# Kernel optimization log

Hardware: AMD Instinct MI355X
Metric: run time of the kernel (lower is better)

The kernel has to match this reference:

```python
import jax, jax.numpy as jnp
import numpy as np

B, O, I, D = 8, 128, 128, 1024


def setup_inputs() -> dict:
    key = jax.random.key(0)
    ks = jax.random.split(key, 10)
    s = 1.0 / np.sqrt(2 * D)  # torch Linear default-ish scale
    return {
        "output": jax.random.normal(ks[0], (B, O, D), jnp.float32),
        "context": jax.random.normal(ks[1], (B, I, D), jnp.float32),
        "mask": jax.random.randint(ks[2], (B, I), 0, 2, jnp.int32),
        # self.w = Linear(2*dim, dim), split into the output-half and context-half
        "w_out_w": jax.random.normal(ks[3], (D, D), jnp.float32) * s,
        "w_ctx_w": jax.random.normal(ks[4], (D, D), jnp.float32) * s,
        "w_b": jax.random.normal(ks[5], (D,), jnp.float32) * s,
        # self.score = Linear(dim, 1)
        "score_w": jax.random.normal(ks[6], (D,), jnp.float32) * (1.0 / np.sqrt(D)),
        "score_b": jnp.zeros((), jnp.float32),
        # self.linear_out = Linear(2*dim, dim)
        "lin_w": jax.random.normal(ks[7], (2 * D, D), jnp.float32) * s,
        "lin_b": jax.random.normal(ks[8], (D,), jnp.float32) * s,
    }


def reference(output, context, mask, w_out_w, w_ctx_w, w_b, score_w, score_b, lin_w, lin_b):
    # Additive (Bahdanau) attention.
    # cat(out, ctx) @ W^T == out @ W1 + ctx @ W2  -> avoid [B,O,I,2D] concat.
    s_out = jnp.einsum('bod,de->boe', output, w_out_w)            # [B,O,D]
    s_ctx = jnp.einsum('bid,de->bie', context, w_ctx_w)           # [B,I,D]
    h = jax.nn.leaky_relu(s_out[:, :, None, :] + s_ctx[:, None, :, :] + w_b)  # [B,O,I,D]
    score = jnp.einsum('boid,d->boi', h, score_w) + score_b       # [B,O,I]
    score = jnp.where(mask[:, None, :] == 1, -jnp.inf, score)
    attn = jax.nn.softmax(score, axis=-1)                         # [B,O,I]
    attn_output = jnp.einsum('boi,bid->bod', attn, context)       # mix=True: bmm
    # fn=True: linear_out on cat(attn_output, output) then leaky_relu
    combined = jnp.concatenate([attn_output, output], axis=-1)    # [B,O,2D]
    attn_output = jax.nn.leaky_relu(combined @ lin_w + lin_b)     # [B,O,D]
    return attn_output, attn
```

## Files before the change

kernel.cpp:

```cpp
#include <hip/hip_runtime.h>

namespace {

constexpr int kB = 8, kO = 128, kI = 128, kD = 1024;
constexpr long kOutAttnOff = (long)kB * kO * kD;

typedef __attribute__((ext_vector_type(8))) short short8;
typedef __attribute__((ext_vector_type(4))) float f32x4;
typedef __attribute__((ext_vector_type(2))) float f32x2;
typedef __attribute__((ext_vector_type(2))) unsigned u32x2;

__device__ __forceinline__ float leaky(float x) { return fmaxf(x, 0.01f * x); }

__device__ __forceinline__ short f2bf(float f) {
    unsigned u = __builtin_bit_cast(unsigned, f);
    u += 0x7FFFu + ((u >> 16) & 1u);
    return (short)(u >> 16);
}
__device__ __forceinline__ void b8tofs(const short8 v, float* f) {
    const unsigned* u = (const unsigned*)&v;
#pragma unroll
    for (int j = 0; j < 4; ++j) {
        f[2 * j]     = __builtin_bit_cast(float, u[j] << 16);
        f[2 * j + 1] = __builtin_bit_cast(float, u[j] & 0xffff0000u);
    }
}
__device__ __forceinline__ void bpair(const short8 a, const short8 b, f32x2* p) {
    float fa[8], fb[8];
    b8tofs(a, fa); b8tofs(b, fb);
#pragma unroll
    for (int j = 0; j < 8; ++j) p[j] = f32x2{fa[j], fb[j]};
}
__device__ __forceinline__ f32x2 vabs2(f32x2 x) {
    u32x2 u = __builtin_bit_cast(u32x2, x);
    u &= 0x7fffffffu;
    return __builtin_bit_cast(f32x2, u);
}

__device__ __forceinline__ void gll16(const void* g, void* l) {
    __builtin_amdgcn_global_load_lds(
        (const __attribute__((address_space(1))) int*)g,
        (__attribute__((address_space(3))) int*)l, 16, 0, 0);
}

__global__ __launch_bounds__(256)
void conv_all(const float* __restrict__ output, const float* __restrict__ context,
              const float* __restrict__ w1, const float* __restrict__ w2,
              const float* __restrict__ lin,
              short* __restrict__ ob16, short* __restrict__ cb16,
              short* __restrict__ w1t, short* __restrict__ w2t,
              short* __restrict__ lint)
{
    __shared__ float T[64][68];
    const int bid = blockIdx.x, tid = threadIdx.x;

    if (bid < 1024) {
        const int idx = bid * 256 + tid;
        const float* src; short* dst; int i;
        if (idx < (1 << 17)) { src = output;  dst = ob16; i = idx; }
        else                 { src = context; dst = cb16; i = idx - (1 << 17); }
        const float4* s4 = (const float4*)src + (long)i * 2;
        const float4 v0 = s4[0], v1 = s4[1];
        short8 r;
        r[0] = f2bf(v0.x); r[1] = f2bf(v0.y); r[2] = f2bf(v0.z); r[3] = f2bf(v0.w);
        r[4] = f2bf(v1.x); r[5] = f2bf(v1.y); r[6] = f2bf(v1.z); r[7] = f2bf(v1.w);
        *(short8*)(dst + (long)i * 8) = r;
        return;
    }

    const int tb = bid - 1024;
    const float* src; short* dst; long C, R; int t2;
    if (tb < 256)      { src = w1;  dst = w1t;  R = 1024; C = 1024; t2 = tb; }
    else if (tb < 512) { src = w2;  dst = w2t;  R = 1024; C = 1024; t2 = tb - 256; }
    else               { src = lin; dst = lint; R = 2048; C = 1024; t2 = tb - 512; }
    const int tr = t2 >> 4, tc = t2 & 15;
    const int r = tid >> 2, q = tid & 3;

    const float* s = src + (long)(tr * 64 + r) * C + tc * 64 + q * 16;
    const float4 a0 = ((const float4*)s)[0];
    const float4 a1 = ((const float4*)s)[1];
    const float4 a2 = ((const float4*)s)[2];
    const float4 a3 = ((const float4*)s)[3];
    *(float4*)&T[r][q * 16 + 0]  = a0;
    *(float4*)&T[r][q * 16 + 4]  = a1;
    *(float4*)&T[r][q * 16 + 8]  = a2;
    *(float4*)&T[r][q * 16 + 12] = a3;
    __syncthreads();

    short8 o0, o1;
#pragma unroll
    for (int j = 0; j < 8; ++j)  o0[j] = f2bf(T[q * 16 + j][r]);
#pragma unroll
    for (int j = 0; j < 8; ++j)  o1[j] = f2bf(T[q * 16 + 8 + j][r]);
    short* dp = dst + (long)(tc * 64 + r) * R + tr * 64 + q * 16;
    *(short8*)dp       = o0;
    *((short8*)dp + 1) = o1;
}

__global__ __launch_bounds__(256, 4)
void mm_jobs(const short* __restrict__ ob16, const short* __restrict__ cb16,
             const short* __restrict__ w1t, const short* __restrict__ w2t,
             const short* __restrict__ lint,
             const float* __restrict__ w_b, const float* __restrict__ lin_b,
             float* __restrict__ s_out, short* __restrict__ s_ctx16,
             float* __restrict__ outlin, short* __restrict__ ctxlin)
{
    __shared__ short As[2][64][64];
    __shared__ short Bs[2][64][64];
    const int tid = threadIdx.x;
    const int t = (blockIdx.x & 7) * 128 + (blockIdx.x >> 3);
    const int lane = tid & 63, w = tid >> 6;

    const short *Ap, *Bp;
    int lda, ldb, bm, bn, ldc;
    const float* bias = nullptr;
    float* Cf = nullptr;
    short* Ch = nullptr;

    if (t < 768) {
        const int job = t >> 8, tl = t & 255;
        bm = (tl & 15) * 64;
        bn = (tl >> 4) * 64;
        lda = 1024; ldb = 1024; ldc = 1024;
        if (job == 0)      { Ap = ob16; Bp = w1t;         bias = w_b;   Cf = s_out;   }
        else if (job == 1) { Ap = ob16; Bp = lint + 1024; ldb = 2048; bias = lin_b; Cf = outlin; }
        else               { Ap = cb16; Bp = w2t;                       Ch = s_ctx16; }
    } else {
        const int tl = t - 768, bz = tl >> 5, t2 = tl & 31;
        bm = (t2 & 15) * 64;
        bn = (t2 >> 4) * 64;
        Ap = lint; lda = 2048;
        Bp = cb16 + (long)bz * (kI * kD); ldb = 1024;
        Ch = ctxlin + (long)bz * (kD * kI); ldc = 128;
    }

    const int m0 = (w >> 1) * 32, n0 = (w & 1) * 32;
    const int fr = lane & 15, fcol = lane >> 4, sl = lane & 7;
    const int r8 = lane >> 3;
    const int sw8 = ((lane & 7) ^ r8) * 8;
    const int w16 = w * 16;

    f32x4 acc[2][2] = {};

    auto stage = [&](int buf, int k0) {
        const short* ga = Ap + (long)(bm + w16 + r8) * lda + k0 + sw8;
        gll16(ga,                 &As[buf][w16][0]);
        gll16(ga + 8 * (long)lda, &As[buf][w16 + 8][0]);
        const short* gb = Bp + (long)(bn + w16 + r8) * ldb + k0 + sw8;
        gll16(gb,                 &Bs[buf][w16][0]);
        gll16(gb + 8 * (long)ldb, &Bs[buf][w16 + 8][0]);
    };

    stage(0, 0);
    __syncthreads();
    int cur = 0;
    for (int s = 0; s < 16; ++s) {
        if (s < 15) stage(cur ^ 1, (s + 1) << 6);
#pragma unroll
        for (int ks8 = 0; ks8 < 8; ks8 += 4) {
            const int sa = ((ks8 + fcol) ^ sl) * 8;
            short8 a[2], b[2];
#pragma unroll
            for (int mi = 0; mi < 2; ++mi)
                a[mi] = *(const short8*)&As[cur][m0 + mi * 16 + fr][sa];
#pragma unroll
            for (int ni = 0; ni < 2; ++ni)
                b[ni] = *(const short8*)&Bs[cur][n0 + ni * 16 + fr][sa];
#pragma unroll
            for (int mi = 0; mi < 2; ++mi)
#pragma unroll
                for (int ni = 0; ni < 2; ++ni)
                    acc[mi][ni] = __builtin_amdgcn_mfma_f32_16x16x32_bf16(
                        a[mi], b[ni], acc[mi][ni], 0, 0, 0);
        }
        __syncthreads();
        cur ^= 1;
    }

    float bv[2] = {0, 0};
    if (bias) {
#pragma unroll
        for (int ni = 0; ni < 2; ++ni) bv[ni] = bias[bn + n0 + ni * 16 + fr];
    }
#pragma unroll
    for (int mi = 0; mi < 2; ++mi)
#pragma unroll
        for (int ni = 0; ni < 2; ++ni)
#pragma unroll
            for (int r = 0; r < 4; ++r) {
                const int row = bm + m0 + mi * 16 + ((lane >> 4) << 2) + r;
                const int col = bn + n0 + ni * 16 + fr;
                const float v = acc[mi][ni][r] + bv[ni];
                if (Ch) Ch[(long)row * ldc + col] = f2bf(v);
                else    Cf[(long)row * ldc + col] = v;
            }
}

__global__ __launch_bounds__(256, 3)
void score_final(const float* __restrict__ s_out, const short* __restrict__ s_ctx16,
                 const float* __restrict__ score_w, const float* __restrict__ score_b,
                 const int* __restrict__ mask, const short* __restrict__ ctxlin,
                 const float* __restrict__ outlin, float* __restrict__ out_main,
                 float* __restrict__ attn_f32)
{
    __shared__ float As[2][1032];
    __shared__ __align__(16) char CsPool[32768];
    __shared__ short Wsh[1032];
    __shared__ float Ps[4][2][128];
    __shared__ float Psi[4][128];
    __shared__ float so_sh[2];
    __shared__ int   Msk[128];
    __shared__ __align__(16) short Pl[16][136];

    short* CsS = (short*)CsPool;
    const int b   = blockIdx.x;
    const int o0  = blockIdx.y * 2;
    const int tid = threadIdx.x;
    const int wv  = tid >> 6;
    const int ln  = tid & 63;
    const int fr  = ln & 15, fg = ln >> 4;

    const short* crow = s_ctx16 + (long)b * kI * kD;
    auto stageCs = [&](int slot, int dc) {
#pragma unroll
        for (int it = 0; it < 4; ++it) {
            const int rb = wv * 32 + it * 8;
            const int r  = rb + (ln >> 3);
            const int sc = (ln & 7) ^ (r & 7);
            gll16(crow + (long)r * kD + dc + sc * 8, CsS + slot * 8192 + rb * 64);
        }
    };

    stageCs(0, 0);

    const float* arow = s_out + (long)(b * kO + o0) * kD;
#pragma unroll
    for (int q = 0; q < 2; ++q) {
        const int tq = tid + q * 256;
        const int rr = tq >> 8, c4 = (tq & 255) * 4;
        *(float4*)&As[rr][c4] = *(const float4*)&arow[(long)rr * kD + c4];
    }
    {
        const float4 w4 = *(const float4*)&score_w[tid * 4];
        const unsigned p0 = (unsigned)(unsigned short)f2bf(w4.x)
                          | ((unsigned)(unsigned short)f2bf(w4.y) << 16);
        const unsigned p1 = (unsigned)(unsigned short)f2bf(w4.z)
                          | ((unsigned)(unsigned short)f2bf(w4.w) << 16);
        *(u32x2*)&Wsh[tid * 4] = u32x2{p0, p1};
    }
    if (tid < 128) Msk[tid] = mask[b * kI + tid];
    {
        short* pf = &Pl[0][0];
        for (int j = tid; j < 272; j += 256) *(short8*)(pf + j * 8) = short8{};
    }
    __syncthreads();

    if (wv < 2) {
        const short8 wA = *(const short8*)&Wsh[ln * 16];
        const short8 wB = *(const short8*)&Wsh[ln * 16 + 8];
        float wf[16];
        b8tofs(wA, wf); b8tofs(wB, wf + 8);
        float acc = 0.0f;
#pragma unroll
        for (int q = 0; q < 4; ++q) {
            const float4 av = *(const float4*)&As[wv][ln * 16 + q * 4];
            acc = fmaf(av.x, wf[q*4+0], acc); acc = fmaf(av.y, wf[q*4+1], acc);
            acc = fmaf(av.z, wf[q*4+2], acc); acc = fmaf(av.w, wf[q*4+3], acc);
        }
#pragma unroll
        for (int d = 1; d < 64; d <<= 1) acc += __shfl_xor(acc, d, 64);
        if (ln == 0) so_sh[wv] = acc;
    }

    f32x2 si2{0.0f, 0.0f};
    f32x2 sa2[2] = {f32x2{0.0f, 0.0f}, f32x2{0.0f, 0.0f}};
    const int kb = wv * 16;

    int buf = 0;
    for (int c = 0; c < 16; ++c) {
        const int dc = c * 64;
        if (c < 15) stageCs(buf ^ 1, dc + 64);
        const short* Cb = CsS + buf * 8192;
        const int sc0 = ((wv * 2 + 0) ^ (ln & 7)) * 8;
        const int sc1 = ((wv * 2 + 1) ^ (ln & 7)) * 8;
        const short8 cA0 = *(const short8*)&Cb[ln * 64 + sc0];
        const short8 cA1 = *(const short8*)&Cb[ln * 64 + sc1];
        const short8 cB0 = *(const short8*)&Cb[(ln + 64) * 64 + sc0];
        const short8 cB1 = *(const short8*)&Cb[(ln + 64) * 64 + sc1];
        f32x2 c2[16];
        bpair(cA0, cB0, c2);
        bpair(cA1, cB1, c2 + 8);
        const short8 w0 = *(const short8*)&Wsh[dc + kb];
        const short8 w1 = *(const short8*)&Wsh[dc + kb + 8];
        float wr[16];
        b8tofs(w0, wr); b8tofs(w1, wr + 8);
        float av0[16], av1[16];
#pragma unroll
        for (int q = 0; q < 4; ++q) {
            *(float4*)&av0[q * 4] = *(const float4*)&As[0][dc + kb + q * 4];
            *(float4*)&av1[q * 4] = *(const float4*)&As[1][dc + kb + q * 4];
        }
#pragma unroll
        for (int d = 0; d < 16; ++d) {
            const f32x2 w2 = {wr[d], wr[d]};
            si2 += c2[d] * w2;
            const f32x2 x0 = c2[d] + f32x2{av0[d], av0[d]};
            const f32x2 x1 = c2[d] + f32x2{av1[d], av1[d]};
            sa2[0] += vabs2(x0) * w2;
            sa2[1] += vabs2(x1) * w2;
        }
        __syncthreads();
        buf ^= 1;
    }

    short* Bsh = (short*)CsPool;
    const short* ctxb = ctxlin + (long)b * (kD * kI);
    auto stageB = [&](int half, int nc) {
#pragma unroll
        for (int it = 0; it < 4; ++it) {
            const int rb = wv * 16 + it * 4;
            const int r  = rb + (ln >> 4);
            const int n  = nc * 64 + r;
            const int sc = (ln & 15) ^ (r & 7);
            gll16(ctxb + (long)n * kI + sc * 8, Bsh + half * 8192 + rb * kI);
        }
    };
    stageB(0, 0);

#pragma unroll
    for (int o = 0; o < 2; ++o) {
        Ps[wv][o][ln]      = sa2[o].x;
        Ps[wv][o][ln + 64] = sa2[o].y;
    }
    Psi[wv][ln]      = si2.x;
    Psi[wv][ln + 64] = si2.y;
    __syncthreads();

    if (wv < 2) {
        const int ow = wv;
        const float negInf = -__builtin_huge_valf();
        const float sb = score_b[0];
        const float siT0 = Psi[0][ln] + Psi[1][ln] + Psi[2][ln] + Psi[3][ln];
        const float siT1 = Psi[0][ln + 64] + Psi[1][ln + 64]
                         + Psi[2][ln + 64] + Psi[3][ln + 64];
        const float saT0 = Ps[0][ow][ln] + Ps[1][ow][ln]
                         + Ps[2][ow][ln] + Ps[3][ow][ln];
        const float saT1 = Ps[0][ow][ln + 64] + Ps[1][ow][ln + 64]
                         + Ps[2][ow][ln + 64] + Ps[3][ow][ln + 64];
        const float soV = so_sh[ow];
        float s0 = 0.505f * (soV + siT0) + 0.495f * saT0 + sb;
        float s1 = 0.505f * (soV + siT1) + 0.495f * saT1 + sb;
        if (Msk[ln]      != 0) s0 = negInf;
        if (Msk[ln + 64] != 0) s1 = negInf;

        float m = fmaxf(s0, s1);
#pragma unroll
        for (int d = 1; d < 64; d <<= 1) m = fmaxf(m, __shfl_xor(m, d, 64));
        const float e0 = __expf(s0 - m);
        const float e1 = __expf(s1 - m);
        float sum = e0 + e1;
#pragma unroll
        for (int d = 1; d < 64; d <<= 1) sum += __shfl_xor(sum, d, 64);
        const float inv = 1.0f / sum;

        const long rowoff = (long)(b * kO + o0 + ow) * kI;
        const float p0 = e0 * inv, p1 = e1 * inv;
        attn_f32[rowoff + ln]      = p0;
        attn_f32[rowoff + ln + 64] = p1;
        Pl[ow][ln]      = f2bf(p0);
        Pl[ow][ln + 64] = f2bf(p1);
    }
    __syncthreads();

    int half = 0;
    for (int nc = 0; nc < 16; ++nc) {
        if (nc < 15) stageB(half ^ 1, nc + 1);
        const short* Bc = Bsh + half * 8192;
        f32x4 acc{};
#pragma unroll
        for (int ks = 0; ks < 4; ++ks) {
            const short8 a = *(const short8*)&Pl[fr][ks * 32 + fg * 8];
            const int sc = ((ks * 4 + fg) ^ (fr & 7)) * 8;
            const short8 bb = *(const short8*)&Bc[(wv * 16 + fr) * kI + sc];
            acc = __builtin_amdgcn_mfma_f32_16x16x32_bf16(a, bb, acc, 0, 0, 0);
        }
        if (fg == 0) {
#pragma unroll
            for (int r = 0; r < 2; ++r) {
                const int n = nc * 64 + wv * 16 + fr;
                const long off = (long)(b * kO + o0 + r) * kD + n;
                out_main[off] = leaky(acc[r] + outlin[off]);
            }
        }
        __syncthreads();
        half ^= 1;
    }
}

}

extern "C" void kernel_launch(void* const* d_in, const int* in_sizes, int n_in,
                              void* d_out, int out_size, void* d_ws, size_t ws_size,
                              hipStream_t stream)
{
    const float* output  = (const float*)d_in[0];
    const float* context = (const float*)d_in[1];
    const int*   mask    = (const int*)d_in[2];
    const float* w_out_w = (const float*)d_in[3];
    const float* w_ctx_w = (const float*)d_in[4];
    const float* w_b     = (const float*)d_in[5];
    const float* score_w = (const float*)d_in[6];
    const float* score_b = (const float*)d_in[7];
    const float* lin_w   = (const float*)d_in[8];
    const float* lin_b   = (const float*)d_in[9];

    float* out_main = (float*)d_out;
    float* out_attn = out_main + kOutAttnOff;
    float* s_out    = out_main;

    char* wp = (char*)d_ws;
    short* s_ctx16 = (short*)wp;  wp += (size_t)2 << 20;
    short* ob16    = (short*)wp;  wp += (size_t)2 << 20;
    short* cb16    = (short*)wp;  wp += (size_t)2 << 20;
    short* w1t     = (short*)wp;  wp += (size_t)2 << 20;
    short* w2t     = (short*)wp;  wp += (size_t)2 << 20;
    short* lint    = (short*)wp;  wp += (size_t)4 << 20;
    float* outlin  = (float*)wp;  wp += (size_t)4 << 20;
    short* ctxlin  = (short*)wp;

    const dim3 blk(256);

    hipLaunchKernelGGL(conv_all, dim3(2048), blk, 0, stream,
        output, context, w_out_w, w_ctx_w, lin_w, ob16, cb16, w1t, w2t, lint);

    hipLaunchKernelGGL(mm_jobs, dim3(1024), blk, 0, stream,
        ob16, cb16, w1t, w2t, lint, w_b, lin_b, s_out, s_ctx16, outlin, ctxlin);

    hipLaunchKernelGGL(score_final, dim3(8, 64), blk, 0, stream,
        s_out, s_ctx16, score_w, score_b, mask, ctxlin, outlin, out_main, out_attn);
}
```

Baseline: 60.90 us.

## Compact unmasked context rows and skip score work for masked positions

Builds a compacted index list of unmasked context positions with ballot and popcount, then gathers only those rows into shared memory. When at most 64 positions are unmasked, a half-width path stages and processes only 64 rows, roughly halving the score-loop loads and FLOPs. Masked scores are set to -inf directly. This adds a ballot pass, an extra barrier and an indirect gather, and the speedup depends on the mask density of the inputs.

After: 61.42 us. Within noise of the previous version (+0.9%).

```diff
diff --git a/kernel.cpp b/kernel.cpp
--- a/kernel.cpp
+++ b/kernel.cpp
@@ -210,6 +210,8 @@
     __shared__ float Psi[4][128];
     __shared__ float so_sh[2];
     __shared__ int   Msk[128];
+    __shared__ unsigned long long Mball[2];
+    __shared__ int   Idx[128];
     __shared__ __align__(16) short Pl[16][136];
 
     short* CsS = (short*)CsPool;
@@ -220,18 +222,12 @@
     const int ln  = tid & 63;
     const int fr  = ln & 15, fg = ln >> 4;
 
-    const short* crow = s_ctx16 + (long)b * kI * kD;
-    auto stageCs = [&](int slot, int dc) {
-#pragma unroll
-        for (int it = 0; it < 4; ++it) {
-            const int rb = wv * 32 + it * 8;
-            const int r  = rb + (ln >> 3);
-            const int sc = (ln & 7) ^ (r & 7);
-            gll16(crow + (long)r * kD + dc + sc * 8, CsS + slot * 8192 + rb * 64);
-        }
-    };
-
-    stageCs(0, 0);
+    int mv = 1;
+    if (tid < 128) { mv = mask[b * kI + tid]; Msk[tid] = mv; }
+    if (wv < 2) {
+        const unsigned long long bal = __ballot(mv == 0);
+        if (ln == 0) Mball[wv] = bal;
+    }
 
     const float* arow = s_out + (long)(b * kO + o0) * kD;
 #pragma unroll
@@ -248,12 +244,47 @@
                           | ((unsigned)(unsigned short)f2bf(w4.w) << 16);
         *(u32x2*)&Wsh[tid * 4] = u32x2{p0, p1};
     }
-    if (tid < 128) Msk[tid] = mask[b * kI + tid];
     {
         short* pf = &Pl[0][0];
         for (int j = tid; j < 272; j += 256) *(short8*)(pf + j * 8) = short8{};
     }
     __syncthreads();
+
+    const unsigned long long m0 = Mball[0], m1 = Mball[1];
+    const int K0 = __popcll(m0);
+    const int K  = K0 + __popcll(m1);
+    if (tid < 128) {
+        if (mv == 0) {
+            const int cp = (tid < 64)
+                ? __popcll(m0 & ((1ull << tid) - 1))
+                : K0 + __popcll(m1 & ((1ull << (tid - 64)) - 1));
+            Idx[cp] = tid;
+        }
+        if (tid >= K) Idx[tid] = 0;
+    }
+    __syncthreads();
+
+    const short* crow = s_ctx16 + (long)b * kI * kD;
+    auto stageCs64 = [&](int slot, int dc) {
+#pragma unroll
+        for (int it = 0; it < 2; ++it) {
+            const int rb = wv * 16 + it * 8;
+            const int r  = rb + (ln >> 3);
+            const int sc = (ln & 7) ^ (r & 7);
+            gll16(crow + (long)Idx[r] * kD + dc + sc * 8, CsS + slot * 8192 + rb * 64);
+        }
+    };
+    auto stageCsF = [&](int slot, int dc) {
+#pragma unroll
+        for (int it = 0; it < 4; ++it) {
+            const int rb = wv * 32 + it * 8;
+            const int r  = rb + (ln >> 3);
+            const int sc = (ln & 7) ^ (r & 7);
+            gll16(crow + (long)Idx[r] * kD + dc + sc * 8, CsS + slot * 8192 + rb * 64);
+        }
+    };
+
+    if (K <= 64) stageCs64(0, 0); else stageCsF(0, 0);
 
     if (wv < 2) {
         const short8 wA = *(const short8*)&Wsh[ln * 16];
@@ -271,46 +302,90 @@
         for (int d = 1; d < 64; d <<= 1) acc += __shfl_xor(acc, d, 64);
         if (ln == 0) so_sh[wv] = acc;
     }
-
-    f32x2 si2{0.0f, 0.0f};
-    f32x2 sa2[2] = {f32x2{0.0f, 0.0f}, f32x2{0.0f, 0.0f}};
+    __syncthreads();
+
     const int kb = wv * 16;
 
-    int buf = 0;
-    for (int c = 0; c < 16; ++c) {
-        const int dc = c * 64;
-        if (c < 15) stageCs(buf ^ 1, dc + 64);
-        const short* Cb = CsS + buf * 8192;
-        const int sc0 = ((wv * 2 + 0) ^ (ln & 7)) * 8;
-        const int sc1 = ((wv * 2 + 1) ^ (ln & 7)) * 8;
-        const short8 cA0 = *(const short8*)&Cb[ln * 64 + sc0];
-        const short8 cA1 = *(const short8*)&Cb[ln * 64 + sc1];
-        const short8 cB0 = *(const short8*)&Cb[(ln + 64) * 64 + sc0];
-        const short8 cB1 = *(const short8*)&Cb[(ln + 64) * 64 + sc1];
-        f32x2 c2[16];
-        bpair(cA0, cB0, c2);
-        bpair(cA1, cB1, c2 + 8);
-        const short8 w0 = *(const short8*)&Wsh[dc + kb];
-        const short8 w1 = *(const short8*)&Wsh[dc + kb + 8];
-        float wr[16];
-        b8tofs(w0, wr); b8tofs(w1, wr + 8);
-        float av0[16], av1[16];
-#pragma unroll
-        for (int q = 0; q < 4; ++q) {
-            *(float4*)&av0[q * 4] = *(const float4*)&As[0][dc + kb + q * 4];
-            *(float4*)&av1[q * 4] = *(const float4*)&As[1][dc + kb + q * 4];
-        }
-#pragma unroll
-        for (int d = 0; d < 16; ++d) {
-            const f32x2 w2 = {wr[d], wr[d]};
-            si2 += c2[d] * w2;
-            const f32x2 x0 = c2[d] + f32x2{av0[d], av0[d]};
-            const f32x2 x1 = c2[d] + f32x2{av1[d], av1[d]};
-            sa2[0] += vabs2(x0) * w2;
-            sa2[1] += vabs2(x1) * w2;
-        }
-        __syncthreads();
-        buf ^= 1;
+    if (K <= 64) {
+        float si = 0.0f, sa0 = 0.0f, sa1 = 0.0f;
+        int buf = 0;
+        for (int c = 0; c < 16; ++c) {
+            const int dc = c * 64;
+            if (c < 15) stageCs64(buf ^ 1, dc + 64);
+            const short* Cb = CsS + buf * 8192;
+            const int sc0 = ((wv * 2 + 0) ^ (ln & 7)) * 8;
+            const int sc1 = ((wv * 2 + 1) ^ (ln & 7)) * 8;
+            const short8 cA0 = *(const short8*)&Cb[ln * 64 + sc0];
+            const short8 cA1 = *(const short8*)&Cb[ln * 64 + sc1];
+            float cf[16];
+            b8tofs(cA0, cf); b8tofs(cA1, cf + 8);
+            const short8 w0 = *(const short8*)&Wsh[dc + kb];
+            const short8 w1 = *(const short8*)&Wsh[dc + kb + 8];
+            float wr[16];
+            b8tofs(w0, wr); b8tofs(w1, wr + 8);
+            float av0[16], av1[16];
+#pragma unroll
+            for (int q = 0; q < 4; ++q) {
+                *(float4*)&av0[q * 4] = *(const float4*)&As[0][dc + kb + q * 4];
+                *(float4*)&av1[q * 4] = *(const float4*)&As[1][dc + kb + q * 4];
+            }
+#pragma unroll
+            for (int d = 0; d < 16; ++d) {
+                si  = fmaf(cf[d], wr[d], si);
+                sa0 = fmaf(__builtin_fabsf(av0[d] + cf[d]), wr[d], sa0);
+                sa1 = fmaf(__builtin_fabsf(av1[d] + cf[d]), wr[d], sa1);
+            }
+            __syncthreads();
+            buf ^= 1;
+        }
+        Psi[wv][ln]    = si;
+        Ps[wv][0][ln]  = sa0;
+        Ps[wv][1][ln]  = sa1;
+    } else {
+        f32x2 si2{0.0f, 0.0f};
+        f32x2 sa2[2] = {f32x2{0.0f, 0.0f}, f32x2{0.0f, 0.0f}};
+        int buf = 0;
+        for (int c = 0; c < 16; ++c) {
+            const int dc = c * 64;
+            if (c < 15) stageCsF(buf ^ 1, dc + 64);
+            const short* Cb = CsS + buf * 8192;
+            const int sc0 = ((wv * 2 + 0) ^ (ln & 7)) * 8;
+            const int sc1 = ((wv * 2 + 1) ^ (ln & 7)) * 8;
+            const short8 cA0 = *(const short8*)&Cb[ln * 64 + sc0];
+            const short8 cA1 = *(const short8*)&Cb[ln * 64 + sc1];
+            const short8 cB0 = *(const short8*)&Cb[(ln + 64) * 64 + sc0];
+            const short8 cB1 = *(const short8*)&Cb[(ln + 64) * 64 + sc1];
+            f32x2 c2[16];
+            bpair(cA0, cB0, c2);
+            bpair(cA1, cB1, c2 + 8);
+            const short8 w0 = *(const short8*)&Wsh[dc + kb];
+            const short8 w1 = *(const short8*)&Wsh[dc + kb + 8];
+            float wr[16];
+            b8tofs(w0, wr); b8tofs(w1, wr + 8);
+            float av0[16], av1[16];
+#pragma unroll
+            for (int q = 0; q < 4; ++q) {
+                *(float4*)&av0[q * 4] = *(const float4*)&As[0][dc + kb + q * 4];
+                *(float4*)&av1[q * 4] = *(const float4*)&As[1][dc + kb + q * 4];
+            }
+#pragma unroll
+            for (int d = 0; d < 16; ++d) {
+                const f32x2 w2 = {wr[d], wr[d]};
+                si2 += c2[d] * w2;
+                const f32x2 x0 = c2[d] + f32x2{av0[d], av0[d]};
+                const f32x2 x1 = c2[d] + f32x2{av1[d], av1[d]};
+                sa2[0] += vabs2(x0) * w2;
+                sa2[1] += vabs2(x1) * w2;
+            }
+            __syncthreads();
+            buf ^= 1;
+        }
+        Psi[wv][ln]         = si2.x;
+        Psi[wv][ln + 64]    = si2.y;
+        Ps[wv][0][ln]       = sa2[0].x;
+        Ps[wv][0][ln + 64]  = sa2[0].y;
+        Ps[wv][1][ln]       = sa2[1].x;
+        Ps[wv][1][ln + 64]  = sa2[1].y;
     }
 
     short* Bsh = (short*)CsPool;
@@ -326,32 +401,28 @@
         }
     };
     stageB(0, 0);
-
-#pragma unroll
-    for (int o = 0; o < 2; ++o) {
-        Ps[wv][o][ln]      = sa2[o].x;
-        Ps[wv][o][ln + 64] = sa2[o].y;
-    }
-    Psi[wv][ln]      = si2.x;
-    Psi[wv][ln + 64] = si2.y;
     __syncthreads();
 
     if (wv < 2) {
         const int ow = wv;
         const float negInf = -__builtin_huge_valf();
         const float sb = score_b[0];
-        const float siT0 = Psi[0][ln] + Psi[1][ln] + Psi[2][ln] + Psi[3][ln];
-        const float siT1 = Psi[0][ln + 64] + Psi[1][ln + 64]
-                         + Psi[2][ln + 64] + Psi[3][ln + 64];
-        const float saT0 = Ps[0][ow][ln] + Ps[1][ow][ln]
-                         + Ps[2][ow][ln] + Ps[3][ow][ln];
-        const float saT1 = Ps[0][ow][ln + 64] + Ps[1][ow][ln + 64]
-                         + Ps[2][ow][ln + 64] + Ps[3][ow][ln + 64];
         const float soV = so_sh[ow];
-        float s0 = 0.505f * (soV + siT0) + 0.495f * saT0 + sb;
-        float s1 = 0.505f * (soV + siT1) + 0.495f * saT1 + sb;
-        if (Msk[ln]      != 0) s0 = negInf;
-        if (Msk[ln + 64] != 0) s1 = negInf;
+        float s0 = negInf, s1 = negInf;
+        if (Msk[ln] == 0) {
+            const int j = __popcll(m0 & ((1ull << ln) - 1));
+            const float siT = Psi[0][j] + Psi[1][j] + Psi[2][j] + Psi[3][j];
+            const float saT = Ps[0][ow][j] + Ps[1][ow][j]
+                            + Ps[2][ow][j] + Ps[3][ow][j];
+            s0 = 0.505f * (soV + siT) + 0.495f * saT + sb;
+        }
+        if (Msk[ln + 64] == 0) {
+            const int j = K0 + __popcll(m1 & ((1ull << ln) - 1));
+            const float siT = Psi[0][j] + Psi[1][j] + Psi[2][j] + Psi[3][j];
+            const float saT = Ps[0][ow][j] + Ps[1][ow][j]
+                            + Ps[2][ow][j] + Ps[3][ow][j];
+            s1 = 0.505f * (soV + siT) + 0.495f * saT + sb;
+        }
 
         float m = fmaxf(s0, s1);
 #pragma unroll
```

## Fuse fp32-to-bf16 conversion and weight transpose into the GEMM kernel

Applied to the files above, without the earlier changes.

Removes the separate conversion/transpose kernel and has the GEMM load fp32 activations and weights directly, converting to bf16 and transposing through a shared-memory staging tile each k-step. This removes a kernel launch and the round-trip of bf16 copies through global memory. In exchange, every GEMM tile re-converts and re-transposes the same weight data many times, and each k-step gains extra syncs plus register-held prefetch in place of async LDS loads. The launch bound also drops to 3 blocks per SIMD.

Result: slower. 77.03 us (+26.5%).

```diff
diff --git a/kernel.cpp b/kernel.cpp
--- a/kernel.cpp
+++ b/kernel.cpp
@@ -36,6 +36,12 @@
     u &= 0x7fffffffu;
     return __builtin_bit_cast(f32x2, u);
 }
+__device__ __forceinline__ short8 pack8(const float4 a, const float4 b) {
+    short8 r;
+    r[0] = f2bf(a.x); r[1] = f2bf(a.y); r[2] = f2bf(a.z); r[3] = f2bf(a.w);
+    r[4] = f2bf(b.x); r[5] = f2bf(b.y); r[6] = f2bf(b.z); r[7] = f2bf(b.w);
+    return r;
+}
 
 __device__ __forceinline__ void gll16(const void* g, void* l) {
     __builtin_amdgcn_global_load_lds(
@@ -43,119 +49,113 @@
         (__attribute__((address_space(3))) int*)l, 16, 0, 0);
 }
 
-__global__ __launch_bounds__(256)
-void conv_all(const float* __restrict__ output, const float* __restrict__ context,
-              const float* __restrict__ w1, const float* __restrict__ w2,
-              const float* __restrict__ lin,
-              short* __restrict__ ob16, short* __restrict__ cb16,
-              short* __restrict__ w1t, short* __restrict__ w2t,
-              short* __restrict__ lint)
-{
-    __shared__ float T[64][68];
-    const int bid = blockIdx.x, tid = threadIdx.x;
-
-    if (bid < 1024) {
-        const int idx = bid * 256 + tid;
-        const float* src; short* dst; int i;
-        if (idx < (1 << 17)) { src = output;  dst = ob16; i = idx; }
-        else                 { src = context; dst = cb16; i = idx - (1 << 17); }
-        const float4* s4 = (const float4*)src + (long)i * 2;
-        const float4 v0 = s4[0], v1 = s4[1];
-        short8 r;
-        r[0] = f2bf(v0.x); r[1] = f2bf(v0.y); r[2] = f2bf(v0.z); r[3] = f2bf(v0.w);
-        r[4] = f2bf(v1.x); r[5] = f2bf(v1.y); r[6] = f2bf(v1.z); r[7] = f2bf(v1.w);
-        *(short8*)(dst + (long)i * 8) = r;
-        return;
-    }
-
-    const int tb = bid - 1024;
-    const float* src; short* dst; long C, R; int t2;
-    if (tb < 256)      { src = w1;  dst = w1t;  R = 1024; C = 1024; t2 = tb; }
-    else if (tb < 512) { src = w2;  dst = w2t;  R = 1024; C = 1024; t2 = tb - 256; }
-    else               { src = lin; dst = lint; R = 2048; C = 1024; t2 = tb - 512; }
-    const int tr = t2 >> 4, tc = t2 & 15;
-    const int r = tid >> 2, q = tid & 3;
-
-    const float* s = src + (long)(tr * 64 + r) * C + tc * 64 + q * 16;
-    const float4 a0 = ((const float4*)s)[0];
-    const float4 a1 = ((const float4*)s)[1];
-    const float4 a2 = ((const float4*)s)[2];
-    const float4 a3 = ((const float4*)s)[3];
-    *(float4*)&T[r][q * 16 + 0]  = a0;
-    *(float4*)&T[r][q * 16 + 4]  = a1;
-    *(float4*)&T[r][q * 16 + 8]  = a2;
-    *(float4*)&T[r][q * 16 + 12] = a3;
-    __syncthreads();
-
-    short8 o0, o1;
-#pragma unroll
-    for (int j = 0; j < 8; ++j)  o0[j] = f2bf(T[q * 16 + j][r]);
-#pragma unroll
-    for (int j = 0; j < 8; ++j)  o1[j] = f2bf(T[q * 16 + 8 + j][r]);
-    short* dp = dst + (long)(tc * 64 + r) * R + tr * 64 + q * 16;
-    *(short8*)dp       = o0;
-    *((short8*)dp + 1) = o1;
-}
-
-__global__ __launch_bounds__(256, 4)
-void mm_jobs(const short* __restrict__ ob16, const short* __restrict__ cb16,
-             const short* __restrict__ w1t, const short* __restrict__ w2t,
-             const short* __restrict__ lint,
-             const float* __restrict__ w_b, const float* __restrict__ lin_b,
-             float* __restrict__ s_out, short* __restrict__ s_ctx16,
-             float* __restrict__ outlin, short* __restrict__ ctxlin)
+__global__ __launch_bounds__(256, 3)
+void mm_all(const float* __restrict__ output, const float* __restrict__ context,
+            const float* __restrict__ w1, const float* __restrict__ w2,
+            const float* __restrict__ lin,
+            const float* __restrict__ w_b, const float* __restrict__ lin_b,
+            float* __restrict__ s_out, short* __restrict__ s_ctx16,
+            float* __restrict__ outlin, short* __restrict__ ctxlin)
 {
     __shared__ short As[2][64][64];
     __shared__ short Bs[2][64][64];
+    __shared__ float Tf[64][65];
+
     const int tid = threadIdx.x;
     const int t = (blockIdx.x & 7) * 128 + (blockIdx.x >> 3);
     const int lane = tid & 63, w = tid >> 6;
 
-    const short *Ap, *Bp;
-    int lda, ldb, bm, bn, ldc;
+    const float *Dsrc, *Tsrc;
+    int R0, C0, bm, bn, ldc;
     const float* bias = nullptr;
     float* Cf = nullptr;
     short* Ch = nullptr;
+    bool transA = false;
 
     if (t < 768) {
         const int job = t >> 8, tl = t & 255;
         bm = (tl & 15) * 64;
         bn = (tl >> 4) * 64;
-        lda = 1024; ldb = 1024; ldc = 1024;
-        if (job == 0)      { Ap = ob16; Bp = w1t;         bias = w_b;   Cf = s_out;   }
-        else if (job == 1) { Ap = ob16; Bp = lint + 1024; ldb = 2048; bias = lin_b; Cf = outlin; }
-        else               { Ap = cb16; Bp = w2t;                       Ch = s_ctx16; }
+        ldc = 1024; R0 = bm; C0 = bn;
+        if (job == 0)      { Dsrc = output;  Tsrc = w1;  bias = w_b;   Cf = s_out;   }
+        else if (job == 1) { Dsrc = output;  Tsrc = lin + (long)1024 * 1024;
+                             bias = lin_b;  Cf = outlin; }
+        else               { Dsrc = context; Tsrc = w2;  Ch = s_ctx16; }
     } else {
         const int tl = t - 768, bz = tl >> 5, t2 = tl & 31;
         bm = (t2 & 15) * 64;
         bn = (t2 >> 4) * 64;
-        Ap = lint; lda = 2048;
-        Bp = cb16 + (long)bz * (kI * kD); ldb = 1024;
+        Dsrc = context + (long)bz * (kI * kD); R0 = bn;
+        Tsrc = lin; C0 = bm;
         Ch = ctxlin + (long)bz * (kD * kI); ldc = 128;
+        transA = true;
     }
 
     const int m0 = (w >> 1) * 32, n0 = (w & 1) * 32;
     const int fr = lane & 15, fcol = lane >> 4, sl = lane & 7;
     const int r8 = lane >> 3;
-    const int sw8 = ((lane & 7) ^ r8) * 8;
+    const int c8 = lane & 7;
     const int w16 = w * 16;
 
     f32x4 acc[2][2] = {};
 
-    auto stage = [&](int buf, int k0) {
-        const short* ga = Ap + (long)(bm + w16 + r8) * lda + k0 + sw8;
-        gll16(ga,                 &As[buf][w16][0]);
-        gll16(ga + 8 * (long)lda, &As[buf][w16 + 8][0]);
-        const short* gb = Bp + (long)(bn + w16 + r8) * ldb + k0 + sw8;
-        gll16(gb,                 &Bs[buf][w16][0]);
-        gll16(gb + 8 * (long)ldb, &Bs[buf][w16 + 8][0]);
-    };
-
-    stage(0, 0);
+    float4 dv[4], tv[4];
+    auto loadDirect = [&](int k0) {
+        const float* g = Dsrc + (long)(R0 + w16 + r8) * kD + k0 + ((c8 ^ r8) * 8);
+        dv[0] = ((const float4*)g)[0];
+        dv[1] = ((const float4*)g)[1];
+        const float* g2 = g + 8 * kD;
+        dv[2] = ((const float4*)g2)[0];
+        dv[3] = ((const float4*)g2)[1];
+    };
+    auto loadTrans = [&](int k0) {
+#pragma unroll
+        for (int p = 0; p < 4; ++p) {
+            const int f = tid + p * 256;
+            const int row = f >> 4, colq = (f & 15) * 4;
+            tv[p] = *(const float4*)&Tsrc[(long)(k0 + row) * 1024 + C0 + colq];
+        }
+    };
+    auto writeDirect = [&](short (*dst)[64]) {
+        *(short8*)&dst[w16 + r8][c8 * 8]     = pack8(dv[0], dv[1]);
+        *(short8*)&dst[w16 + 8 + r8][c8 * 8] = pack8(dv[2], dv[3]);
+    };
+    auto writeTf = [&]() {
+#pragma unroll
+        for (int p = 0; p < 4; ++p) {
+            const int f = tid + p * 256;
+            const int row = f >> 4, colq = (f & 15) * 4;
+            Tf[row][colq + 0] = tv[p].x;
+            Tf[row][colq + 1] = tv[p].y;
+            Tf[row][colq + 2] = tv[p].z;
+            Tf[row][colq + 3] = tv[p].w;
+        }
+    };
+    auto transToDst = [&](short (*dst)[64]) {
+#pragma unroll
+        for (int h = 0; h < 2; ++h) {
+            const int n = w16 + h * 8 + r8;
+            const int kc = (c8 ^ r8) * 8;
+            float4 a, b;
+            a.x = Tf[kc + 0][n]; a.y = Tf[kc + 1][n];
+            a.z = Tf[kc + 2][n]; a.w = Tf[kc + 3][n];
+            b.x = Tf[kc + 4][n]; b.y = Tf[kc + 5][n];
+            b.z = Tf[kc + 6][n]; b.w = Tf[kc + 7][n];
+            *(short8*)&dst[n][c8 * 8] = pack8(a, b);
+        }
+    };
+
+    loadDirect(0);
+    loadTrans(0);
+    writeTf();
+    writeDirect(transA ? Bs[0] : As[0]);
     __syncthreads();
+    transToDst(transA ? As[0] : Bs[0]);
+    __syncthreads();
+
     int cur = 0;
     for (int s = 0; s < 16; ++s) {
-        if (s < 15) stage(cur ^ 1, (s + 1) << 6);
+        if (s < 15) { loadDirect((s + 1) << 6); loadTrans((s + 1) << 6); }
 #pragma unroll
         for (int ks8 = 0; ks8 < 8; ks8 += 4) {
             const int sa = ((ks8 + fcol) ^ sl) * 8;
@@ -173,8 +173,16 @@
                     acc[mi][ni] = __builtin_amdgcn_mfma_f32_16x16x32_bf16(
                         a[mi], b[ni], acc[mi][ni], 0, 0, 0);
         }
-        __syncthreads();
-        cur ^= 1;
+        if (s < 15) {
+            const int nxt = cur ^ 1;
+            __syncthreads();
+            writeTf();
+            writeDirect(transA ? Bs[nxt] : As[nxt]);
+            __syncthreads();
+            transToDst(transA ? As[nxt] : Bs[nxt]);
+            __syncthreads();
+            cur = nxt;
+        }
     }
 
     float bv[2] = {0, 0};
@@ -420,21 +428,14 @@
 
     char* wp = (char*)d_ws;
     short* s_ctx16 = (short*)wp;  wp += (size_t)2 << 20;
-    short* ob16    = (short*)wp;  wp += (size_t)2 << 20;
-    short* cb16    = (short*)wp;  wp += (size_t)2 << 20;
-    short* w1t     = (short*)wp;  wp += (size_t)2 << 20;
-    short* w2t     = (short*)wp;  wp += (size_t)2 << 20;
-    short* lint    = (short*)wp;  wp += (size_t)4 << 20;
     float* outlin  = (float*)wp;  wp += (size_t)4 << 20;
     short* ctxlin  = (short*)wp;
 
     const dim3 blk(256);
 
-    hipLaunchKernelGGL(conv_all, dim3(2048), blk, 0, stream,
-        output, context, w_out_w, w_ctx_w, lin_w, ob16, cb16, w1t, w2t, lint);
-
-    hipLaunchKernelGGL(mm_jobs, dim3(1024), blk, 0, stream,
-        ob16, cb16, w1t, w2t, lint, w_b, lin_b, s_out, s_ctx16, outlin, ctxlin);
+    hipLaunchKernelGGL(mm_all, dim3(1024), blk, 0, stream,
+        output, context, w_out_w, w_ctx_w, lin_w, w_b, lin_b,
+        s_out, s_ctx16, outlin, ctxlin);
 
     hipLaunchKernelGGL(score_final, dim3(8, 64), blk, 0, stream,
         s_out, s_ctx16, score_w, score_b, mask, ctxlin, outlin, out_main, out_attn);
```
